# Performance work log

Hardware: AMD Instinct MI355X
Metric: run time of the kernel (lower is better)

Reference implementation:

```python
import jax, jax.numpy as jnp
import numpy as np

B, S, R, C_IN = 1, 1024, 512, 256   # batch, n_seq (MSA rows), n_res, rep1d_extra_feat
H, CH = 8, 32                       # num_heads, attention_num_c (H*CH == C_IN)


def setup_inputs() -> dict:
    key = jax.random.key(0)
    ks = jax.random.split(key, 7)
    scale = 0.02
    return {
        "x1d": jax.random.normal(ks[0], (B, S, R, C_IN), jnp.float32),
        "mask": jnp.ones((B, S, R), jnp.float32),
        "ln_scale": jnp.ones((C_IN,), jnp.float32),
        "ln_bias": jnp.zeros((C_IN,), jnp.float32),
        "Wq": jax.random.normal(ks[1], (C_IN, H * CH), jnp.float32) * scale,
        "Wk": jax.random.normal(ks[2], (C_IN, CH), jnp.float32) * scale,
        "Wv": jax.random.normal(ks[3], (C_IN, CH), jnp.float32) * scale,
        "Wg": jax.random.normal(ks[4], (C_IN, H * CH), jnp.float32) * scale,
        "bg": jnp.zeros((H * CH,), jnp.float32),
        "Wf": jax.random.normal(ks[5], (H * CH, C_IN), jnpp := jnp.float32) * scale if False else jax.random.normal(ks[5], (H * CH, C_IN), jnp.float32) * scale,
        "bf": jnp.zeros((C_IN,), jnp.float32),
    }


def reference(x1d, mask, ln_scale, ln_bias, Wq, Wk, Wv, Wg, bg, Wf, bf):
    # transpose so attention runs over the MSA-row (column) axis
    x = jnp.swapaxes(x1d, -2, -3)          # [B, R, S, C_IN]
    m = jnp.swapaxes(mask, -1, -2)         # [B, R, S]
    # LayerNorm (eps matches torch default 1e-5)
    mu = jnp.mean(x, axis=-1, keepdims=True)
    var = jnp.mean((x - mu) ** 2, axis=-1, keepdims=True)
    xn = (x - mu) * jax.lax.rsqrt(var + 1e-5) * ln_scale + ln_bias
    # masked mean over rows -> global query
    q_avg = jnp.sum(xn * m[..., None], axis=-2) / (jnp.sum(m, axis=-1)[..., None] + 1e-10)  # [B,R,C_IN]
    att_bias = (1e9 * (m - 1.0))[..., None, :]                         # [B,R,1,S]
    q = (q_avg @ Wq).reshape(*q_avg.shape[:-1], H, CH) * (CH ** -0.5)  # [B,R,H,CH]
    k = xn @ Wk                                                        # [B,R,S,CH]
    v = xn @ Wv                                                        # [B,R,S,CH]
    gate = jax.nn.sigmoid(xn @ Wg + bg).reshape(*xn.shape[:-1], H, CH)  # [B,R,S,H,CH]
    w = jax.nn.softmax(jnp.einsum('brhc,brsc->brhs', q, k) + att_bias, axis=-1)  # [B,R,H,S]
    o = jnp.einsum('brhs,brsc->brhc', w, v)                            # [B,R,H,CH]
    o = o[..., None, :, :] * gate                                      # [B,R,S,H,CH]
    out = o.reshape(*o.shape[:-2], H * CH) @ Wf + bf                   # [B,R,S,C_IN]
    return jnp.swapaxes(out, -2, -3)                                   # [B,S,R,C_IN]
```

## Files before the change

kernel.cpp:

```cpp
#include <hip/hip_runtime.h>
#include <hip/hip_bf16.h>

#define S_DIM 1024
#define R_DIM 512
#define C_DIM 256
#define BS 64
#define SB (S_DIM / BS)

#define XN_OFF (16u << 20)
#define XN_BYTES (512ull * 1024ull * 256ull * 2ull)

typedef __attribute__((ext_vector_type(8))) short short8;
typedef __attribute__((ext_vector_type(8))) unsigned short ushort8v;
typedef __attribute__((ext_vector_type(4))) unsigned short ushort4v;
typedef __attribute__((ext_vector_type(4))) float floatx4;

__device__ inline float bf2f(unsigned short u) {
    return __uint_as_float(((unsigned int)u) << 16);
}
__device__ inline unsigned short f2bf(float f) {
    unsigned int x = __float_as_uint(f);
    unsigned int r = ((x >> 16) & 1u) + 0x7fffu;
    return (unsigned short)((x + r) >> 16);
}

__device__ inline float fast_rcp(float x) {
    float r;
    asm volatile("v_rcp_f32 %0, %1" : "=v"(r) : "v"(x));
    return r;
}

__device__ inline void nt_stf(float* p, float v) {
    __builtin_nontemporal_store(v, p);
}

__device__ inline void async16nt(unsigned short* lds, const unsigned short* g) {
    __builtin_amdgcn_global_load_lds(
        (const __attribute__((address_space(1))) void*)g,
        (__attribute__((address_space(3))) void*)lds, 16, 0, 2);
}

__global__ __launch_bounds__(256) void prep_kernel(
        const float* __restrict__ Wk, const float* __restrict__ Wv,
        const float* __restrict__ Wg, const float* __restrict__ Wf,
        unsigned short* __restrict__ wgT, unsigned short* __restrict__ wfhi,
        unsigned short* __restrict__ wflo, unsigned short* __restrict__ wkvT) {
    int b = blockIdx.x;
    int k = threadIdx.x;
    wgT[b * 256 + k] = f2bf(Wg[k * 256 + b]);
    float w = Wf[k * 256 + b];
    unsigned short hi = f2bf(w);
    wfhi[b * 256 + k] = hi;
    wflo[b * 256 + k] = f2bf(w - bf2f(hi));
    if (b < 64) {
        float t = (b < 32) ? Wk[k * 32 + b] : Wv[k * 32 + (b - 32)];
        wkvT[b * 256 + k] = f2bf(t);
    }
}

template <int CACHE>
__device__ inline void stage_xn(const float* __restrict__ x,
                                const float* __restrict__ lns,
                                const float* __restrict__ lnb,
                                int s0, int r, unsigned short* xn,
                                unsigned short* __restrict__ xnws) {
    const int t = threadIdx.x;
    const int row = t >> 2;
    const int q = t & 3;
    const size_t base = ((size_t)(s0 + row) * R_DIM + r) * C_DIM + q * 64;
    const floatx4* gp = reinterpret_cast<const floatx4*>(x + base);
    floatx4 v[16];
    float sum = 0.f, sq = 0.f;
#pragma unroll
    for (int i = 0; i < 16; i++) {
        v[i] = gp[i];
        sum += v[i][0] + v[i][1] + v[i][2] + v[i][3];
        sq  += v[i][0] * v[i][0] + v[i][1] * v[i][1] + v[i][2] * v[i][2] + v[i][3] * v[i][3];
    }
    sum += __shfl_xor(sum, 1); sq += __shfl_xor(sq, 1);
    sum += __shfl_xor(sum, 2); sq += __shfl_xor(sq, 2);
    float mu = sum * (1.f / 256.f);
    float var = sq * (1.f / 256.f) - mu * mu;
    float rs = rsqrtf(var + 1e-5f);
    const floatx4* sp = reinterpret_cast<const floatx4*>(lns + q * 64);
    const floatx4* bp = reinterpret_cast<const floatx4*>(lnb + q * 64);
    unsigned short* wp = xn + row * 264 + q * 64;
    unsigned short* gw = CACHE ? (xnws + ((size_t)(s0 + row) * R_DIM + r) * C_DIM + q * 64)
                               : nullptr;
#pragma unroll
    for (int i = 0; i < 16; i += 2) {
        floatx4 g0 = sp[i],     b0 = bp[i];
        floatx4 g1 = sp[i + 1], b1 = bp[i + 1];
        ushort8v u;
        u[0] = f2bf((v[i][0]     - mu) * rs * g0[0] + b0[0]);
        u[1] = f2bf((v[i][1]     - mu) * rs * g0[1] + b0[1]);
        u[2] = f2bf((v[i][2]     - mu) * rs * g0[2] + b0[2]);
        u[3] = f2bf((v[i][3]     - mu) * rs * g0[3] + b0[3]);
        u[4] = f2bf((v[i + 1][0] - mu) * rs * g1[0] + b1[0]);
        u[5] = f2bf((v[i + 1][1] - mu) * rs * g1[1] + b1[1]);
        u[6] = f2bf((v[i + 1][2] - mu) * rs * g1[2] + b1[2]);
        u[7] = f2bf((v[i + 1][3] - mu) * rs * g1[3] + b1[3]);
        *reinterpret_cast<ushort8v*>(wp + i * 4) = u;
        if (CACHE) *reinterpret_cast<ushort8v*>(gw + i * 4) = u;
    }
}

template <int CACHE>
__global__ __launch_bounds__(256, 4) void k1_kernel(
        const float* __restrict__ x, const float* __restrict__ mask,
        const float* __restrict__ lns, const float* __restrict__ lnb,
        const unsigned short* __restrict__ wkvT, unsigned short* __restrict__ kv,
        float* __restrict__ qsum, float* __restrict__ msum,
        unsigned short* __restrict__ xnws) {
    __shared__ unsigned short xn[64 * 264];
    __shared__ float mk[64];
    const int sblk = blockIdx.x, r = blockIdx.y;
    const int s0 = sblk * BS;
    const int t = threadIdx.x;
    stage_xn<CACHE>(x, lns, lnb, s0, r, xn, xnws);
    if (t < 64) mk[t] = mask[(size_t)(s0 + t) * R_DIM + r];
    __syncthreads();

    const int w = t >> 6, l = t & 63;
    const int lr = l & 15, lk = (l >> 4) * 8;
    floatx4 acc[4] = {};
    const unsigned short* arow = xn + (w * 16 + lr) * 264;
#pragma unroll
    for (int kk = 0; kk < 256; kk += 32) {
        short8 a = *reinterpret_cast<const short8*>(arow + kk + lk);
#pragma unroll
        for (int n = 0; n < 4; n++) {
            short8 b = *reinterpret_cast<const short8*>(wkvT + (n * 16 + lr) * 256 + kk + lk);
            acc[n] = __builtin_amdgcn_mfma_f32_16x16x32_bf16(a, b, acc[n], 0, 0, 0);
        }
    }
    unsigned short* kvp = kv + ((size_t)r * S_DIM + s0) * 64;
#pragma unroll
    for (int n = 0; n < 4; n++) {
        int col = n * 16 + lr;
#pragma unroll
        for (int i = 0; i < 4; i++) {
            int row = w * 16 + (l >> 4) * 4 + i;
            kvp[(size_t)row * 64 + col] = f2bf(acc[n][i]);
        }
    }
    float cs = 0.f;
    const int c = t;
#pragma unroll 8
    for (int row = 0; row < 64; row++) cs += bf2f(xn[row * 264 + c]) * mk[row];
    qsum[((size_t)r * SB + sblk) * 256 + c] = cs;
    if (t < 64) {
        float m = mk[t];
#pragma unroll
        for (int off = 32; off; off >>= 1) m += __shfl_xor(m, off);
        if (t == 0) msum[r * SB + sblk] = m;
    }
}

__global__ __launch_bounds__(256) void k2_kernel(
        const float* __restrict__ mask, const float* __restrict__ Wq,
        const float* __restrict__ qsum, const float* __restrict__ msum,
        const unsigned short* __restrict__ kv, float* __restrict__ oout) {
    __shared__ float qavg[256];
    __shared__ float qh[256];
    __shared__ float lg[8][1024];
    __shared__ float red[8];
    __shared__ unsigned short vt[256 * 36];
    const int r = blockIdx.x;
    const int t = threadIdx.x;

    float ms = 0.f;
#pragma unroll
    for (int i = 0; i < SB; i++) ms += msum[r * SB + i];
    float inv = 1.f / (ms + 1e-10f);
    float qs = 0.f;
#pragma unroll
    for (int i = 0; i < SB; i++) qs += qsum[((size_t)r * SB + i) * 256 + t];
    qavg[t] = qs * inv;
    __syncthreads();

    float accq = 0.f;
#pragma unroll 8
    for (int c = 0; c < 256; c++) accq += qavg[c] * Wq[c * 256 + t];
    qh[t] = accq * 0.17677669529663687f;
    __syncthreads();

    const unsigned short* kvr = kv + (size_t)r * S_DIM * 64;
#pragma unroll
    for (int i = 0; i < 4; i++) {
        int s = i * 256 + t;
        float bias = 1e9f * (mask[(size_t)s * R_DIM + r] - 1.f);
        const unsigned int* kp = reinterpret_cast<const unsigned int*>(kvr + (size_t)s * 64);
        float kvals[32];
#pragma unroll
        for (int j = 0; j < 16; j++) {
            unsigned int u = kp[j];
            kvals[2 * j]     = __uint_as_float(u << 16);
            kvals[2 * j + 1] = __uint_as_float(u & 0xffff0000u);
        }
#pragma unroll
        for (int h = 0; h < 8; h++) {
            float d = 0.f;
#pragma unroll
            for (int ch = 0; ch < 32; ch++) d += qh[h * 32 + ch] * kvals[ch];
            lg[h][s] = d + bias;
        }
    }
    __syncthreads();

    for (int h = 0; h < 8; h++) {
        float mx = -1e30f;
#pragma unroll
        for (int i = 0; i < 4; i++) mx = fmaxf(mx, lg[h][i * 256 + t]);
        for (int off = 32; off; off >>= 1) mx = fmaxf(mx, __shfl_xor(mx, off));
        if ((t & 63) == 0) red[t >> 6] = mx;
        __syncthreads();
        mx = fmaxf(fmaxf(red[0], red[1]), fmaxf(red[2], red[3]));
        float sm = 0.f;
#pragma unroll
        for (int i = 0; i < 4; i++) {
            float e = __expf(lg[h][i * 256 + t] - mx);
            lg[h][i * 256 + t] = e;
            sm += e;
        }
        for (int off = 32; off; off >>= 1) sm += __shfl_xor(sm, off);
        if ((t & 63) == 0) red[4 + (t >> 6)] = sm;
        __syncthreads();
        sm = red[4] + red[5] + red[6] + red[7];
        float isv = 1.f / sm;
#pragma unroll
        for (int i = 0; i < 4; i++) lg[h][i * 256 + t] *= isv;
        __syncthreads();
    }

    const int h = t >> 5, ch = t & 31;
    float o = 0.f;
    for (int st = 0; st < 4; st++) {
        __syncthreads();
        {
            const unsigned short* src = kvr + ((size_t)(st * 256 + t)) * 64 + 32;
            ushort4v* dst = reinterpret_cast<ushort4v*>(vt + t * 36);
#pragma unroll
            for (int j = 0; j < 8; j++)
                dst[j] = *reinterpret_cast<const ushort4v*>(src + 4 * j);
        }
        __syncthreads();
#pragma unroll 8
        for (int sl = 0; sl < 256; sl++)
            o += lg[h][sl + st * 256] * bf2f(vt[sl * 36 + ch]);
    }
    oout[r * 256 + t] = o;
}

__global__ __launch_bounds__(256, 4) void k3r_kernel(
        const float* __restrict__ x, const float* __restrict__ lns,
        const float* __restrict__ lnb, const unsigned short* __restrict__ wgT,
        const unsigned short* __restrict__ wfhi, const unsigned short* __restrict__ wflo,
        const float* __restrict__ oin, const float* __restrict__ bg,
        const float* __restrict__ bfv, float* __restrict__ out) {
    __shared__ unsigned short xa[64 * 264];
    const int sblk = blockIdx.x, r = blockIdx.y;
    const int s0 = sblk * BS;
    const int t = threadIdx.x;
    stage_xn<0>(x, lns, lnb, s0, r, xa, nullptr);
    __syncthreads();

    const int w = t >> 6, l = t & 63;
    const int lr = l & 15, lk4 = (l >> 4);
    const int colbase = w * 64;

    float bgv[4], ov[4];
#pragma unroll
    for (int n = 0; n < 4; n++) {
        int col = colbase + n * 16 + lr;
        bgv[n] = bg[col];
        ov[n] = oin[r * 256 + col];
    }

    floatx4 acc[4][4] = {};
#pragma unroll
    for (int kk = 0; kk < 256; kk += 32) {
        short8 a[4];
#pragma unroll
        for (int m = 0; m < 4; m++)
            a[m] = *reinterpret_cast<const short8*>(xa + (m * 16 + lr) * 264 + kk + lk4 * 8);
#pragma unroll
        for (int n = 0; n < 4; n++) {
            short8 b = *reinterpret_cast<const short8*>(wgT + (size_t)(colbase + n * 16 + lr) * 256 + kk + lk4 * 8);
#pragma unroll
            for (int m = 0; m < 4; m++)
                acc[m][n] = __builtin_amdgcn_mfma_f32_16x16x32_bf16(a[m], b, acc[m][n], 0, 0, 0);
        }
    }
    __syncthreads();

#pragma unroll
    for (int m = 0; m < 4; m++) {
#pragma unroll
        for (int n = 0; n < 4; n++) {
            int col = colbase + n * 16 + lr;
#pragma unroll
            for (int i = 0; i < 4; i++) {
                int row = m * 16 + lk4 * 4 + i;
                float e = __expf(-(acc[m][n][i] + bgv[n]));
                float g = fast_rcp(1.f + e);
                xa[row * 264 + col] = f2bf(g * ov[n]);
            }
        }
    }
    __syncthreads();

    floatx4 acc2[4][4] = {};
#pragma unroll
    for (int kk = 0; kk < 256; kk += 32) {
        short8 ah[4];
#pragma unroll
        for (int m = 0; m < 4; m++)
            ah[m] = *reinterpret_cast<const short8*>(xa + (m * 16 + lr) * 264 + kk + lk4 * 8);
#pragma unroll
        for (int n = 0; n < 4; n++) {
            const size_t boff = (size_t)(colbase + n * 16 + lr) * 256 + kk + lk4 * 8;
            short8 bh = *reinterpret_cast<const short8*>(wfhi + boff);
            short8 bl = *reinterpret_cast<const short8*>(wflo + boff);
#pragma unroll
            for (int m = 0; m < 4; m++) {
                acc2[m][n] = __builtin_amdgcn_mfma_f32_16x16x32_bf16(ah[m], bh, acc2[m][n], 0, 0, 0);
                acc2[m][n] = __builtin_amdgcn_mfma_f32_16x16x32_bf16(ah[m], bl, acc2[m][n], 0, 0, 0);
            }
        }
    }

#pragma unroll
    for (int n = 0; n < 4; n++) {
        int col = colbase + n * 16 + lr;
        float bfc = bfv[col];
#pragma unroll
        for (int m = 0; m < 4; m++) {
#pragma unroll
            for (int i = 0; i < 4; i++) {
                int row = m * 16 + lk4 * 4 + i;
                out[((size_t)(s0 + row) * R_DIM + r) * C_DIM + col] = acc2[m][n][i] + bfc;
            }
        }
    }
}

__global__ __launch_bounds__(256, 2) void k3c_kernel(
        const unsigned short* __restrict__ xnws, const unsigned short* __restrict__ wgT,
        const unsigned short* __restrict__ wfhi, const unsigned short* __restrict__ wflo,
        const float* __restrict__ oin, const float* __restrict__ bg,
        const float* __restrict__ bfv, float* __restrict__ out) {
    __shared__ unsigned short xa[2][64 * 256];
    const int sblk = blockIdx.x, r = blockIdx.y;
    const int s0 = sblk * 128;
    const int t = threadIdx.x;
    const int w = t >> 6, l = t & 63;

    {
        const int c1 = l & 31;
        const int rh = l >> 5;
#pragma unroll
        for (int T = 0; T < 2; T++)
#pragma unroll
            for (int j = 0; j < 8; j++) {
                int row = w * 16 + 2 * j + rh;
                size_t src = ((size_t)(s0 + T * 64 + row) * R_DIM + r) * C_DIM
                             + (size_t)((c1 ^ (row & 7)) * 8);
                async16nt(&xa[T][(w * 16 + 2 * j) * 256], xnws + src);
            }
    }

    const int lr = l & 15, lk4 = (l >> 4);
    const int colbase = w * 64;
    const int sw = lr & 7;

    float bgv[4], ov[4], bfc[4];
#pragma unroll
    for (int n = 0; n < 4; n++) {
        int col = colbase + n * 16 + lr;
        bgv[n] = bg[col];
        ov[n] = oin[r * 256 + col];
        bfc[n] = bfv[col];
    }
    __syncthreads();

    floatx4 acc[2][4][4] = {};
    {
        const unsigned short* wgb = wgT + (size_t)(colbase + lr) * 256 + lk4 * 8;
        short8 cw[4], nw[4];
#pragma unroll
        for (int n = 0; n < 4; n++)
            cw[n] = *reinterpret_cast<const short8*>(wgb + n * 4096);
#pragma unroll
        for (int kk = 0; kk < 256; kk += 32) {
            if (kk < 224) {
#pragma unroll
                for (int n = 0; n < 4; n++)
                    nw[n] = *reinterpret_cast<const short8*>(wgb + n * 4096 + kk + 32);
            }
            const int ch = (((kk >> 3) + lk4) ^ sw) * 8;
#pragma unroll
            for (int T = 0; T < 2; T++) {
                short8 a[4];
#pragma unroll
                for (int m = 0; m < 4; m++)
                    a[m] = *reinterpret_cast<const short8*>(&xa[T][(m * 16 + lr) * 256 + ch]);
#pragma unroll
                for (int n = 0; n < 4; n++)
#pragma unroll
                    for (int m = 0; m < 4; m++)
                        acc[T][m][n] = __builtin_amdgcn_mfma_f32_16x16x32_bf16(a[m], cw[n], acc[T][m][n], 0, 0, 0);
            }
            if (kk < 224) {
#pragma unroll
                for (int n = 0; n < 4; n++) cw[n] = nw[n];
            }
        }
    }
    __syncthreads();

#pragma unroll
    for (int T = 0; T < 2; T++)
#pragma unroll
    for (int m = 0; m < 4; m++) {
#pragma unroll
        for (int n = 0; n < 4; n++) {
            int col = colbase + n * 16 + lr;
#pragma unroll
            for (int i = 0; i < 4; i++) {
                int row = m * 16 + lk4 * 4 + i;
                float e = __expf(-(acc[T][m][n][i] + bgv[n]));
                float g = fast_rcp(1.f + e);
                int idx = row * 256 + (((col >> 3) ^ (row & 7)) * 8) + (col & 7);
                xa[T][idx] = f2bf(g * ov[n]);
            }
        }
    }
    __syncthreads();

    floatx4 acc2[2][4][4] = {};
    {
        const unsigned short* whb = wfhi + (size_t)(colbase + lr) * 256 + lk4 * 8;
        const unsigned short* wlb = wflo + (size_t)(colbase + lr) * 256 + lk4 * 8;
        short8 chw[4], clw[4], nhw[4], nlw[4];
#pragma unroll
        for (int n = 0; n < 4; n++) {
            chw[n] = *reinterpret_cast<const short8*>(whb + n * 4096);
            clw[n] = *reinterpret_cast<const short8*>(wlb + n * 4096);
        }
#pragma unroll
        for (int kk = 0; kk < 256; kk += 32) {
            if (kk < 224) {
#pragma unroll
                for (int n = 0; n < 4; n++) {
                    nhw[n] = *reinterpret_cast<const short8*>(whb + n * 4096 + kk + 32);
                    nlw[n] = *reinterpret_cast<const short8*>(wlb + n * 4096 + kk + 32);
                }
            }
            const int ch = (((kk >> 3) + lk4) ^ sw) * 8;
#pragma unroll
            for (int T = 0; T < 2; T++) {
                short8 ah[4];
#pragma unroll
                for (int m = 0; m < 4; m++)
                    ah[m] = *reinterpret_cast<const short8*>(&xa[T][(m * 16 + lr) * 256 + ch]);
#pragma unroll
                for (int n = 0; n < 4; n++)
#pragma unroll
                    for (int m = 0; m < 4; m++) {
                        acc2[T][m][n] = __builtin_amdgcn_mfma_f32_16x16x32_bf16(ah[m], chw[n], acc2[T][m][n], 0, 0, 0);
                        acc2[T][m][n] = __builtin_amdgcn_mfma_f32_16x16x32_bf16(ah[m], clw[n], acc2[T][m][n], 0, 0, 0);
                    }
            }
            if (kk < 224) {
#pragma unroll
                for (int n = 0; n < 4; n++) { chw[n] = nhw[n]; clw[n] = nlw[n]; }
            }
        }
    }

#pragma unroll
    for (int T = 0; T < 2; T++)
#pragma unroll
    for (int n = 0; n < 4; n++) {
        int col = colbase + n * 16 + lr;
#pragma unroll
        for (int m = 0; m < 4; m++) {
#pragma unroll
            for (int i = 0; i < 4; i++) {
                int row = T * 64 + m * 16 + lk4 * 4 + i;
                nt_stf(out + ((size_t)(s0 + row) * R_DIM + r) * C_DIM + col, acc2[T][m][n][i] + bfc[n]);
            }
        }
    }
}

extern "C" void kernel_launch(void* const* d_in, const int* in_sizes, int n_in,
                              void* d_out, int out_size, void* d_ws, size_t ws_size,
                              hipStream_t stream) {
    const float* x1   = (const float*)d_in[0];
    const float* mask = (const float*)d_in[1];
    const float* lns  = (const float*)d_in[2];
    const float* lnb  = (const float*)d_in[3];
    const float* Wq   = (const float*)d_in[4];
    const float* Wk   = (const float*)d_in[5];
    const float* Wv   = (const float*)d_in[6];
    const float* Wg   = (const float*)d_in[7];
    const float* bg   = (const float*)d_in[8];
    const float* Wf   = (const float*)d_in[9];
    const float* bfv  = (const float*)d_in[10];

    char* ws = (char*)d_ws;
    unsigned short* wgT  = (unsigned short*)(ws);
    unsigned short* wfhi = (unsigned short*)(ws + 131072);
    unsigned short* wflo = (unsigned short*)(ws + 262144);
    unsigned short* wkvT = (unsigned short*)(ws + 393216);
    float* qsum = (float*)(ws + 425984);
    float* msum = (float*)(ws + 425984 + 8388608);
    float* oo   = (float*)(ws + 425984 + 8388608 + 32768);
    unsigned short* xnws = (unsigned short*)(ws + XN_OFF);
    unsigned short* kv = (unsigned short*)d_out;
    float* out = (float*)d_out;

    const bool big_ws = ws_size >= (size_t)XN_OFF + (size_t)XN_BYTES;

    prep_kernel<<<256, 256, 0, stream>>>(Wk, Wv, Wg, Wf, wgT, wfhi, wflo, wkvT);
    if (big_ws) {
        k1_kernel<1><<<dim3(SB, R_DIM), 256, 0, stream>>>(x1, mask, lns, lnb, wkvT, kv, qsum, msum, xnws);
        k2_kernel<<<R_DIM, 256, 0, stream>>>(mask, Wq, qsum, msum, kv, oo);
        k3c_kernel<<<dim3(SB / 2, R_DIM), 256, 0, stream>>>(xnws, wgT, wfhi, wflo, oo, bg, bfv, out);
    } else {
        k1_kernel<0><<<dim3(SB, R_DIM), 256, 0, stream>>>(x1, mask, lns, lnb, wkvT, kv, qsum, msum, nullptr);
        k2_kernel<<<R_DIM, 256, 0, stream>>>(mask, Wq, qsum, msum, kv, oo);
        k3r_kernel<<<dim3(SB, R_DIM), 256, 0, stream>>>(x1, lns, lnb, wgT, wfhi, wflo, oo, bg, bfv, out);
    }
}
```

Before: 783.0 us.

## Make k1 persistent over eight row tiles with register prefetch and warp specialization

k1 now launches 2x512 blocks of 512 threads instead of 16x512 blocks of 256. Each block loops over eight 64-row tiles and prefetches the next tile's x into registers while processing the current one. Within a tile, half the threads run the MFMA K/V projection and the other half compute the masked column sums, so the two no longer run back to back. This trades fewer blocks and fewer waves per SM, plus higher register pressure from double buffering, for overlap of global loads with compute. The shared stage_xn helper is inlined into k3r.

```diff
diff --git a/kernel.cpp b/kernel.cpp
--- a/kernel.cpp
+++ b/kernel.cpp
@@ -59,54 +59,7 @@
 }
 
 template <int CACHE>
-__device__ inline void stage_xn(const float* __restrict__ x,
-                                const float* __restrict__ lns,
-                                const float* __restrict__ lnb,
-                                int s0, int r, unsigned short* xn,
-                                unsigned short* __restrict__ xnws) {
-    const int t = threadIdx.x;
-    const int row = t >> 2;
-    const int q = t & 3;
-    const size_t base = ((size_t)(s0 + row) * R_DIM + r) * C_DIM + q * 64;
-    const floatx4* gp = reinterpret_cast<const floatx4*>(x + base);
-    floatx4 v[16];
-    float sum = 0.f, sq = 0.f;
-#pragma unroll
-    for (int i = 0; i < 16; i++) {
-        v[i] = gp[i];
-        sum += v[i][0] + v[i][1] + v[i][2] + v[i][3];
-        sq  += v[i][0] * v[i][0] + v[i][1] * v[i][1] + v[i][2] * v[i][2] + v[i][3] * v[i][3];
-    }
-    sum += __shfl_xor(sum, 1); sq += __shfl_xor(sq, 1);
-    sum += __shfl_xor(sum, 2); sq += __shfl_xor(sq, 2);
-    float mu = sum * (1.f / 256.f);
-    float var = sq * (1.f / 256.f) - mu * mu;
-    float rs = rsqrtf(var + 1e-5f);
-    const floatx4* sp = reinterpret_cast<const floatx4*>(lns + q * 64);
-    const floatx4* bp = reinterpret_cast<const floatx4*>(lnb + q * 64);
-    unsigned short* wp = xn + row * 264 + q * 64;
-    unsigned short* gw = CACHE ? (xnws + ((size_t)(s0 + row) * R_DIM + r) * C_DIM + q * 64)
-                               : nullptr;
-#pragma unroll
-    for (int i = 0; i < 16; i += 2) {
-        floatx4 g0 = sp[i],     b0 = bp[i];
-        floatx4 g1 = sp[i + 1], b1 = bp[i + 1];
-        ushort8v u;
-        u[0] = f2bf((v[i][0]     - mu) * rs * g0[0] + b0[0]);
-        u[1] = f2bf((v[i][1]     - mu) * rs * g0[1] + b0[1]);
-        u[2] = f2bf((v[i][2]     - mu) * rs * g0[2] + b0[2]);
-        u[3] = f2bf((v[i][3]     - mu) * rs * g0[3] + b0[3]);
-        u[4] = f2bf((v[i + 1][0] - mu) * rs * g1[0] + b1[0]);
-        u[5] = f2bf((v[i + 1][1] - mu) * rs * g1[1] + b1[1]);
-        u[6] = f2bf((v[i + 1][2] - mu) * rs * g1[2] + b1[2]);
-        u[7] = f2bf((v[i + 1][3] - mu) * rs * g1[3] + b1[3]);
-        *reinterpret_cast<ushort8v*>(wp + i * 4) = u;
-        if (CACHE) *reinterpret_cast<ushort8v*>(gw + i * 4) = u;
-    }
-}
-
-template <int CACHE>
-__global__ __launch_bounds__(256, 4) void k1_kernel(
+__global__ __launch_bounds__(512, 4) void k1_kernel(
         const float* __restrict__ x, const float* __restrict__ mask,
         const float* __restrict__ lns, const float* __restrict__ lnb,
         const unsigned short* __restrict__ wkvT, unsigned short* __restrict__ kv,
@@ -114,46 +67,107 @@
         unsigned short* __restrict__ xnws) {
     __shared__ unsigned short xn[64 * 264];
     __shared__ float mk[64];
-    const int sblk = blockIdx.x, r = blockIdx.y;
-    const int s0 = sblk * BS;
+    const int bx = blockIdx.x, r = blockIdx.y;
     const int t = threadIdx.x;
-    stage_xn<CACHE>(x, lns, lnb, s0, r, xn, xnws);
-    if (t < 64) mk[t] = mask[(size_t)(s0 + t) * R_DIM + r];
-    __syncthreads();
-
-    const int w = t >> 6, l = t & 63;
-    const int lr = l & 15, lk = (l >> 4) * 8;
-    floatx4 acc[4] = {};
-    const unsigned short* arow = xn + (w * 16 + lr) * 264;
-#pragma unroll
-    for (int kk = 0; kk < 256; kk += 32) {
-        short8 a = *reinterpret_cast<const short8*>(arow + kk + lk);
-#pragma unroll
-        for (int n = 0; n < 4; n++) {
-            short8 b = *reinterpret_cast<const short8*>(wkvT + (n * 16 + lr) * 256 + kk + lk);
-            acc[n] = __builtin_amdgcn_mfma_f32_16x16x32_bf16(a, b, acc[n], 0, 0, 0);
-        }
-    }
-    unsigned short* kvp = kv + ((size_t)r * S_DIM + s0) * 64;
-#pragma unroll
-    for (int n = 0; n < 4; n++) {
-        int col = n * 16 + lr;
-#pragma unroll
-        for (int i = 0; i < 4; i++) {
-            int row = w * 16 + (l >> 4) * 4 + i;
-            kvp[(size_t)row * 64 + col] = f2bf(acc[n][i]);
-        }
-    }
-    float cs = 0.f;
-    const int c = t;
+    const int row = t >> 3;
+    const int q = t & 7;
+
+    floatx4 va[8], vb[8];
+    {
+        const floatx4* gp = reinterpret_cast<const floatx4*>(
+            x + ((size_t)((bx * 8 + 0) * 64 + row) * R_DIM + r) * C_DIM + q * 32);
+#pragma unroll
+        for (int i = 0; i < 8; i++) va[i] = gp[i];
+    }
+
+    auto body = [&](int it, floatx4* vc, floatx4* vn) {
+        const int s0 = (bx * 8 + it) * 64;
+        if (it < 7) {
+            const floatx4* gp = reinterpret_cast<const floatx4*>(
+                x + ((size_t)(s0 + 64 + row) * R_DIM + r) * C_DIM + q * 32);
+#pragma unroll
+            for (int i = 0; i < 8; i++) vn[i] = gp[i];
+        }
+        if (t < 64) mk[t] = mask[(size_t)(s0 + t) * R_DIM + r];
+        float sum = 0.f, sq = 0.f;
+#pragma unroll
+        for (int i = 0; i < 8; i++) {
+            sum += vc[i][0] + vc[i][1] + vc[i][2] + vc[i][3];
+            sq  += vc[i][0] * vc[i][0] + vc[i][1] * vc[i][1]
+                 + vc[i][2] * vc[i][2] + vc[i][3] * vc[i][3];
+        }
+        sum += __shfl_xor(sum, 1); sq += __shfl_xor(sq, 1);
+        sum += __shfl_xor(sum, 2); sq += __shfl_xor(sq, 2);
+        sum += __shfl_xor(sum, 4); sq += __shfl_xor(sq, 4);
+        float mu = sum * (1.f / 256.f);
+        float var = sq * (1.f / 256.f) - mu * mu;
+        float rs = rsqrtf(var + 1e-5f);
+        const floatx4* sp = reinterpret_cast<const floatx4*>(lns + q * 32);
+        const floatx4* bp = reinterpret_cast<const floatx4*>(lnb + q * 32);
+        unsigned short* wp = xn + row * 264 + q * 32;
+        unsigned short* gw = CACHE ? (xnws + ((size_t)(s0 + row) * R_DIM + r) * C_DIM + q * 32)
+                                   : nullptr;
+#pragma unroll
+        for (int i = 0; i < 8; i += 2) {
+            floatx4 g0 = sp[i],     b0 = bp[i];
+            floatx4 g1 = sp[i + 1], b1 = bp[i + 1];
+            ushort8v u;
+            u[0] = f2bf((vc[i][0]     - mu) * rs * g0[0] + b0[0]);
+            u[1] = f2bf((vc[i][1]     - mu) * rs * g0[1] + b0[1]);
+            u[2] = f2bf((vc[i][2]     - mu) * rs * g0[2] + b0[2]);
+            u[3] = f2bf((vc[i][3]     - mu) * rs * g0[3] + b0[3]);
+            u[4] = f2bf((vc[i + 1][0] - mu) * rs * g1[0] + b1[0]);
+            u[5] = f2bf((vc[i + 1][1] - mu) * rs * g1[1] + b1[1]);
+            u[6] = f2bf((vc[i + 1][2] - mu) * rs * g1[2] + b1[2]);
+            u[7] = f2bf((vc[i + 1][3] - mu) * rs * g1[3] + b1[3]);
+            *reinterpret_cast<ushort8v*>(wp + i * 4) = u;
+            if (CACHE) *reinterpret_cast<ushort8v*>(gw + i * 4) = u;
+        }
+        __syncthreads();
+
+        if (t < 256) {
+            const int w = t >> 6, l = t & 63;
+            const int lr = l & 15, lk = (l >> 4) * 8;
+            floatx4 acc[4] = {};
+            const unsigned short* arow = xn + (w * 16 + lr) * 264;
+#pragma unroll
+            for (int kk = 0; kk < 256; kk += 32) {
+                short8 a = *reinterpret_cast<const short8*>(arow + kk + lk);
+#pragma unroll
+                for (int n = 0; n < 4; n++) {
+                    short8 b = *reinterpret_cast<const short8*>(wkvT + (n * 16 + lr) * 256 + kk + lk);
+                    acc[n] = __builtin_amdgcn_mfma_f32_16x16x32_bf16(a, b, acc[n], 0, 0, 0);
+                }
+            }
+            unsigned short* kvp = kv + ((size_t)r * S_DIM + s0) * 64;
+#pragma unroll
+            for (int n = 0; n < 4; n++) {
+                int col = n * 16 + lr;
+#pragma unroll
+                for (int i = 0; i < 4; i++) {
+                    int rw = w * 16 + (l >> 4) * 4 + i;
+                    kvp[(size_t)rw * 64 + col] = f2bf(acc[n][i]);
+                }
+            }
+        } else {
+            const int c = t - 256;
+            float cs = 0.f;
 #pragma unroll 8
-    for (int row = 0; row < 64; row++) cs += bf2f(xn[row * 264 + c]) * mk[row];
-    qsum[((size_t)r * SB + sblk) * 256 + c] = cs;
-    if (t < 64) {
-        float m = mk[t];
-#pragma unroll
-        for (int off = 32; off; off >>= 1) m += __shfl_xor(m, off);
-        if (t == 0) msum[r * SB + sblk] = m;
+            for (int rw = 0; rw < 64; rw++) cs += bf2f(xn[rw * 264 + c]) * mk[rw];
+            qsum[((size_t)r * SB + (bx * 8 + it)) * 256 + c] = cs;
+            if (t < 320) {
+                float m = mk[t - 256];
+#pragma unroll
+                for (int off = 32; off; off >>= 1) m += __shfl_xor(m, off);
+                if (t == 256) msum[r * SB + (bx * 8 + it)] = m;
+            }
+        }
+        __syncthreads();
+    };
+
+    for (int it = 0; it < 8; it += 2) {
+        body(it, va, vb);
+        body(it + 1, vb, va);
     }
 }
 
@@ -262,7 +276,43 @@
     const int sblk = blockIdx.x, r = blockIdx.y;
     const int s0 = sblk * BS;
     const int t = threadIdx.x;
-    stage_xn<0>(x, lns, lnb, s0, r, xa, nullptr);
+    {
+        const int row = t >> 2;
+        const int q = t & 3;
+        const size_t base = ((size_t)(s0 + row) * R_DIM + r) * C_DIM + q * 64;
+        const floatx4* gp = reinterpret_cast<const floatx4*>(x + base);
+        floatx4 v[16];
+        float sum = 0.f, sq = 0.f;
+#pragma unroll
+        for (int i = 0; i < 16; i++) {
+            v[i] = gp[i];
+            sum += v[i][0] + v[i][1] + v[i][2] + v[i][3];
+            sq  += v[i][0] * v[i][0] + v[i][1] * v[i][1] + v[i][2] * v[i][2] + v[i][3] * v[i][3];
+        }
+        sum += __shfl_xor(sum, 1); sq += __shfl_xor(sq, 1);
+        sum += __shfl_xor(sum, 2); sq += __shfl_xor(sq, 2);
+        float mu = sum * (1.f / 256.f);
+        float var = sq * (1.f / 256.f) - mu * mu;
+        float rs = rsqrtf(var + 1e-5f);
+        const floatx4* sp = reinterpret_cast<const floatx4*>(lns + q * 64);
+        const floatx4* bp = reinterpret_cast<const floatx4*>(lnb + q * 64);
+        unsigned short* wp = xa + row * 264 + q * 64;
+#pragma unroll
+        for (int i = 0; i < 16; i += 2) {
+            floatx4 g0 = sp[i],     b0 = bp[i];
+            floatx4 g1 = sp[i + 1], b1 = bp[i + 1];
+            ushort8v u;
+            u[0] = f2bf((v[i][0]     - mu) * rs * g0[0] + b0[0]);
+            u[1] = f2bf((v[i][1]     - mu) * rs * g0[1] + b0[1]);
+            u[2] = f2bf((v[i][2]     - mu) * rs * g0[2] + b0[2]);
+            u[3] = f2bf((v[i][3]     - mu) * rs * g0[3] + b0[3]);
+            u[4] = f2bf((v[i + 1][0] - mu) * rs * g1[0] + b1[0]);
+            u[5] = f2bf((v[i + 1][1] - mu) * rs * g1[1] + b1[1]);
+            u[6] = f2bf((v[i + 1][2] - mu) * rs * g1[2] + b1[2]);
+            u[7] = f2bf((v[i + 1][3] - mu) * rs * g1[3] + b1[3]);
+            *reinterpret_cast<ushort8v*>(wp + i * 4) = u;
+        }
+    }
     __syncthreads();
 
     const int w = t >> 6, l = t & 63;
@@ -526,11 +576,11 @@
 
     prep_kernel<<<256, 256, 0, stream>>>(Wk, Wv, Wg, Wf, wgT, wfhi, wflo, wkvT);
     if (big_ws) {
-        k1_kernel<1><<<dim3(SB, R_DIM), 256, 0, stream>>>(x1, mask, lns, lnb, wkvT, kv, qsum, msum, xnws);
+        k1_kernel<1><<<dim3(2, R_DIM), 512, 0, stream>>>(x1, mask, lns, lnb, wkvT, kv, qsum, msum, xnws);
         k2_kernel<<<R_DIM, 256, 0, stream>>>(mask, Wq, qsum, msum, kv, oo);
         k3c_kernel<<<dim3(SB / 2, R_DIM), 256, 0, stream>>>(xnws, wgT, wfhi, wflo, oo, bg, bfv, out);
     } else {
-        k1_kernel<0><<<dim3(SB, R_DIM), 256, 0, stream>>>(x1, mask, lns, lnb, wkvT, kv, qsum, msum, nullptr);
+        k1_kernel<0><<<dim3(2, R_DIM), 512, 0, stream>>>(x1, mask, lns, lnb, wkvT, kv, qsum, msum, nullptr);
         k2_kernel<<<R_DIM, 256, 0, stream>>>(mask, Wq, qsum, msum, kv, oo);
         k3r_kernel<<<dim3(SB, R_DIM), 256, 0, stream>>>(x1, lns, lnb, wgT, wfhi, wflo, oo, bg, bfv, out);
     }
```

Result: slower. 904.3 us (+15.5%).

## Split LayerNorm into a contiguous streaming pass before K/V projection

Applied to the files above, without the earlier changes.

The first stage is split in two. A new kernel LayerNorms x in its natural contiguous order, so each block covers 32 consecutive (s,r) rows, and writes bf16 xn to the workspace. A second kernel then loads xn tiles into XOR-swizzled shared memory with async copies and runs the K/V MFMA, masked q-sum and mask-sum. This replaces the strided per-column fp32 reads of x with fully coalesced streaming. The cost is an extra launch, plus re-reading the bf16 xn with strided 512-byte rows.

```diff
diff --git a/kernel.cpp b/kernel.cpp
--- a/kernel.cpp
+++ b/kernel.cpp
@@ -58,37 +58,34 @@
     }
 }
 
-template <int CACHE>
-__device__ inline void stage_xn(const float* __restrict__ x,
-                                const float* __restrict__ lns,
-                                const float* __restrict__ lnb,
-                                int s0, int r, unsigned short* xn,
-                                unsigned short* __restrict__ xnws) {
+__global__ __launch_bounds__(256, 4) void k1a_kernel(
+        const float* __restrict__ x, const float* __restrict__ lns,
+        const float* __restrict__ lnb, unsigned short* __restrict__ xnws) {
     const int t = threadIdx.x;
-    const int row = t >> 2;
-    const int q = t & 3;
-    const size_t base = ((size_t)(s0 + row) * R_DIM + r) * C_DIM + q * 64;
+    const int row = t >> 3;
+    const int q = t & 7;
+    const size_t base = ((size_t)blockIdx.x * 32 + row) * 256 + q * 32;
     const floatx4* gp = reinterpret_cast<const floatx4*>(x + base);
-    floatx4 v[16];
+    floatx4 v[8];
     float sum = 0.f, sq = 0.f;
 #pragma unroll
-    for (int i = 0; i < 16; i++) {
+    for (int i = 0; i < 8; i++) {
         v[i] = gp[i];
         sum += v[i][0] + v[i][1] + v[i][2] + v[i][3];
-        sq  += v[i][0] * v[i][0] + v[i][1] * v[i][1] + v[i][2] * v[i][2] + v[i][3] * v[i][3];
+        sq  += v[i][0] * v[i][0] + v[i][1] * v[i][1]
+             + v[i][2] * v[i][2] + v[i][3] * v[i][3];
     }
     sum += __shfl_xor(sum, 1); sq += __shfl_xor(sq, 1);
     sum += __shfl_xor(sum, 2); sq += __shfl_xor(sq, 2);
+    sum += __shfl_xor(sum, 4); sq += __shfl_xor(sq, 4);
     float mu = sum * (1.f / 256.f);
     float var = sq * (1.f / 256.f) - mu * mu;
     float rs = rsqrtf(var + 1e-5f);
-    const floatx4* sp = reinterpret_cast<const floatx4*>(lns + q * 64);
-    const floatx4* bp = reinterpret_cast<const floatx4*>(lnb + q * 64);
-    unsigned short* wp = xn + row * 264 + q * 64;
-    unsigned short* gw = CACHE ? (xnws + ((size_t)(s0 + row) * R_DIM + r) * C_DIM + q * 64)
-                               : nullptr;
-#pragma unroll
-    for (int i = 0; i < 16; i += 2) {
+    const floatx4* sp = reinterpret_cast<const floatx4*>(lns + q * 32);
+    const floatx4* bp = reinterpret_cast<const floatx4*>(lnb + q * 32);
+    unsigned short* gw = xnws + base;
+#pragma unroll
+    for (int i = 0; i < 8; i += 2) {
         floatx4 g0 = sp[i],     b0 = bp[i];
         floatx4 g1 = sp[i + 1], b1 = bp[i + 1];
         ushort8v u;
@@ -100,24 +97,122 @@
         u[5] = f2bf((v[i + 1][1] - mu) * rs * g1[1] + b1[1]);
         u[6] = f2bf((v[i + 1][2] - mu) * rs * g1[2] + b1[2]);
         u[7] = f2bf((v[i + 1][3] - mu) * rs * g1[3] + b1[3]);
-        *reinterpret_cast<ushort8v*>(wp + i * 4) = u;
-        if (CACHE) *reinterpret_cast<ushort8v*>(gw + i * 4) = u;
-    }
-}
-
-template <int CACHE>
-__global__ __launch_bounds__(256, 4) void k1_kernel(
+        *reinterpret_cast<ushort8v*>(gw + i * 4) = u;
+    }
+}
+
+__global__ __launch_bounds__(256, 4) void k1b_kernel(
+        const unsigned short* __restrict__ xnws, const float* __restrict__ mask,
+        const unsigned short* __restrict__ wkvT, unsigned short* __restrict__ kv,
+        float* __restrict__ qsum, float* __restrict__ msum) {
+    __shared__ unsigned short xn[64 * 256];
+    __shared__ float mk[64];
+    const int sblk = blockIdx.x, r = blockIdx.y;
+    const int s0 = sblk * BS;
+    const int t = threadIdx.x;
+    const int w = t >> 6, l = t & 63;
+
+    {
+        const int c1 = l & 31;
+        const int rh = l >> 5;
+#pragma unroll
+        for (int j = 0; j < 8; j++) {
+            int row = w * 16 + 2 * j + rh;
+            size_t src = ((size_t)(s0 + row) * R_DIM + r) * C_DIM
+                         + (size_t)((c1 ^ (row & 7)) * 8);
+            async16nt(xn + (w * 16 + 2 * j) * 256, xnws + src);
+        }
+    }
+    if (t < 64) mk[t] = mask[(size_t)(s0 + t) * R_DIM + r];
+    __syncthreads();
+
+    const int lr = l & 15, lk4 = l >> 4;
+    const int sw = lr & 7;
+    floatx4 acc[4] = {};
+#pragma unroll
+    for (int kk = 0; kk < 256; kk += 32) {
+        const int ch = (((kk >> 3) + lk4) ^ sw) * 8;
+        short8 a = *reinterpret_cast<const short8*>(xn + (w * 16 + lr) * 256 + ch);
+#pragma unroll
+        for (int n = 0; n < 4; n++) {
+            short8 b = *reinterpret_cast<const short8*>(wkvT + (n * 16 + lr) * 256 + kk + lk4 * 8);
+            acc[n] = __builtin_amdgcn_mfma_f32_16x16x32_bf16(a, b, acc[n], 0, 0, 0);
+        }
+    }
+    unsigned short* kvp = kv + ((size_t)r * S_DIM + s0) * 64;
+#pragma unroll
+    for (int n = 0; n < 4; n++) {
+        int col = n * 16 + lr;
+#pragma unroll
+        for (int i = 0; i < 4; i++) {
+            int row = w * 16 + lk4 * 4 + i;
+            kvp[(size_t)row * 64 + col] = f2bf(acc[n][i]);
+        }
+    }
+    {
+        const int c = t;
+        const int chi = c >> 3, clo = c & 7;
+        float cs = 0.f;
+#pragma unroll 8
+        for (int row = 0; row < 64; row++)
+            cs += bf2f(xn[row * 256 + ((chi ^ (row & 7)) * 8 + clo)]) * mk[row];
+        qsum[((size_t)r * SB + sblk) * 256 + c] = cs;
+    }
+    if (t < 64) {
+        float m = mk[t];
+#pragma unroll
+        for (int off = 32; off; off >>= 1) m += __shfl_xor(m, off);
+        if (t == 0) msum[r * SB + sblk] = m;
+    }
+}
+
+__global__ __launch_bounds__(256, 4) void k1_old_kernel(
         const float* __restrict__ x, const float* __restrict__ mask,
         const float* __restrict__ lns, const float* __restrict__ lnb,
         const unsigned short* __restrict__ wkvT, unsigned short* __restrict__ kv,
-        float* __restrict__ qsum, float* __restrict__ msum,
-        unsigned short* __restrict__ xnws) {
+        float* __restrict__ qsum, float* __restrict__ msum) {
     __shared__ unsigned short xn[64 * 264];
     __shared__ float mk[64];
     const int sblk = blockIdx.x, r = blockIdx.y;
     const int s0 = sblk * BS;
     const int t = threadIdx.x;
-    stage_xn<CACHE>(x, lns, lnb, s0, r, xn, xnws);
+    {
+        const int row = t >> 2;
+        const int q = t & 3;
+        const size_t base = ((size_t)(s0 + row) * R_DIM + r) * C_DIM + q * 64;
+        const floatx4* gp = reinterpret_cast<const floatx4*>(x + base);
+        floatx4 v[16];
+        float sum = 0.f, sq = 0.f;
+#pragma unroll
+        for (int i = 0; i < 16; i++) {
+            v[i] = gp[i];
+            sum += v[i][0] + v[i][1] + v[i][2] + v[i][3];
+            sq  += v[i][0] * v[i][0] + v[i][1] * v[i][1] + v[i][2] * v[i][2] + v[i][3] * v[i][3];
+        }
+        sum += __shfl_xor(sum, 1); sq += __shfl_xor(sq, 1);
+        sum += __shfl_xor(sum, 2); sq += __shfl_xor(sq, 2);
+        float mu = sum * (1.f / 256.f);
+        float var = sq * (1.f / 256.f) - mu * mu;
+        float rs = rsqrtf(var + 1e-5f);
+        const floatx4* sp = reinterpret_cast<const floatx4*>(lns + q * 64);
+        const floatx4* bp = reinterpret_cast<const floatx4*>(lnb + q * 64);
+        unsigned short* wp = xn + row * 264 + q * 64;
+#pragma unroll
+        for (int i = 0; i < 16; i += 2) {
+            floatx4 g0 = sp[i],     b0 = bp[i];
+            floatx4 g1 = sp[i + 1], b1 = bp[i + 1];
+            ushort8v u;
+            u[0] = f2bf((v[i][0]     - mu) * rs * g0[0] + b0[0]);
+            u[1] = f2bf((v[i][1]     - mu) * rs * g0[1] + b0[1]);
+            u[2] = f2bf((v[i][2]     - mu) * rs * g0[2] + b0[2]);
+            u[3] = f2bf((v[i][3]     - mu) * rs * g0[3] + b0[3]);
+            u[4] = f2bf((v[i + 1][0] - mu) * rs * g1[0] + b1[0]);
+            u[5] = f2bf((v[i + 1][1] - mu) * rs * g1[1] + b1[1]);
+            u[6] = f2bf((v[i + 1][2] - mu) * rs * g1[2] + b1[2]);
+            u[7] = f2bf((v[i + 1][3] - mu) * rs * g1[3] + b1[3]);
+            *reinterpret_cast<ushort8v*>(wp + i * 4) = u;
+        }
+    }
     if (t < 64) mk[t] = mask[(size_t)(s0 + t) * R_DIM + r];
     __syncthreads();
 
@@ -262,7 +357,43 @@
     const int sblk = blockIdx.x, r = blockIdx.y;
     const int s0 = sblk * BS;
     const int t = threadIdx.x;
-    stage_xn<0>(x, lns, lnb, s0, r, xa, nullptr);
+    {
+        const int row = t >> 2;
+        const int q = t & 3;
+        const size_t base = ((size_t)(s0 + row) * R_DIM + r) * C_DIM + q * 64;
+        const floatx4* gp = reinterpret_cast<const floatx4*>(x + base);
+        floatx4 v[16];
+        float sum = 0.f, sq = 0.f;
+#pragma unroll
+        for (int i = 0; i < 16; i++) {
+            v[i] = gp[i];
+            sum += v[i][0] + v[i][1] + v[i][2] + v[i][3];
+            sq  += v[i][0] * v[i][0] + v[i][1] * v[i][1] + v[i][2] * v[i][2] + v[i][3] * v[i][3];
+        }
+        sum += __shfl_xor(sum, 1); sq += __shfl_xor(sq, 1);
+        sum += __shfl_xor(sum, 2); sq += __shfl_xor(sq, 2);
+        float mu = sum * (1.f / 256.f);
+        float var = sq * (1.f / 256.f) - mu * mu;
+        float rs = rsqrtf(var + 1e-5f);
+        const floatx4* sp = reinterpret_cast<const floatx4*>(lns + q * 64);
+        const floatx4* bp = reinterpret_cast<const floatx4*>(lnb + q * 64);
+        unsigned short* wp = xa + row * 264 + q * 64;
+#pragma unroll
+        for (int i = 0; i < 16; i += 2) {
+            floatx4 g0 = sp[i],     b0 = bp[i];
+            floatx4 g1 = sp[i + 1], b1 = bp[i + 1];
+            ushort8v u;
+            u[0] = f2bf((v[i][0]     - mu) * rs * g0[0] + b0[0]);
+            u[1] = f2bf((v[i][1]     - mu) * rs * g0[1] + b0[1]);
+            u[2] = f2bf((v[i][2]     - mu) * rs * g0[2] + b0[2]);
+            u[3] = f2bf((v[i][3]     - mu) * rs * g0[3] + b0[3]);
+            u[4] = f2bf((v[i + 1][0] - mu) * rs * g1[0] + b1[0]);
+            u[5] = f2bf((v[i + 1][1] - mu) * rs * g1[1] + b1[1]);
+            u[6] = f2bf((v[i + 1][2] - mu) * rs * g1[2] + b1[2]);
+            u[7] = f2bf((v[i + 1][3] - mu) * rs * g1[3] + b1[3]);
+            *reinterpret_cast<ushort8v*>(wp + i * 4) = u;
+        }
+    }
     __syncthreads();
 
     const int w = t >> 6, l = t & 63;
@@ -526,11 +657,12 @@
 
     prep_kernel<<<256, 256, 0, stream>>>(Wk, Wv, Wg, Wf, wgT, wfhi, wflo, wkvT);
     if (big_ws) {
-        k1_kernel<1><<<dim3(SB, R_DIM), 256, 0, stream>>>(x1, mask, lns, lnb, wkvT, kv, qsum, msum, xnws);
+        k1a_kernel<<<(S_DIM * R_DIM) / 32, 256, 0, stream>>>(x1, lns, lnb, xnws);
+        k1b_kernel<<<dim3(SB, R_DIM), 256, 0, stream>>>(xnws, mask, wkvT, kv, qsum, msum);
         k2_kernel<<<R_DIM, 256, 0, stream>>>(mask, Wq, qsum, msum, kv, oo);
         k3c_kernel<<<dim3(SB / 2, R_DIM), 256, 0, stream>>>(xnws, wgT, wfhi, wflo, oo, bg, bfv, out);
     } else {
-        k1_kernel<0><<<dim3(SB, R_DIM), 256, 0, stream>>>(x1, mask, lns, lnb, wkvT, kv, qsum, msum, nullptr);
+        k1_old_kernel<<<dim3(SB, R_DIM), 256, 0, stream>>>(x1, mask, lns, lnb, wkvT, kv, qsum, msum);
         k2_kernel<<<R_DIM, 256, 0, stream>>>(mask, Wq, qsum, msum, kv, oo);
         k3r_kernel<<<dim3(SB, R_DIM), 256, 0, stream>>>(x1, lns, lnb, wgT, wfhi, wflo, oo, bg, bfv, out);
     }
```

After: 801.3 us. 1.02x slower.
